# Kernel optimization log

Hardware: AMD Instinct MI355X
Metric: run time of the kernel (lower is better)

Reference implementation:

```python
import jax, jax.numpy as jnp
import numpy as np

B, N, DM = 4, 1024, 256
DEPTH, D_STATE, D_CONV, EXPAND = 12, 16, 4, 2
D_INNER = EXPAND * DM
DT_RANK = (DM + 15) // 16
MASKED = 256            # fixed number of masked tokens per row (CLS never masked)
MAX_VIS = N - MASKED    # static visible length -> jit-safe gather/pad
EPS = 1e-5


def setup_inputs() -> dict:
    key = jax.random.key(0)
    ks = jax.random.split(key, 8)
    tokens = jax.random.normal(ks[0], (B, N, DM), jnp.float32)
    # mask: exactly MASKED random positions True per row, among first N-1 (CLS visible)
    def row_mask(k):
        perm = jax.random.permutation(k, N - 1)
        return jnp.zeros((N,), bool).at[perm[:MASKED]].set(True)
    mask = jax.vmap(row_mask)(jax.random.split(ks[1], B))
    sc = 0.02
    L = DEPTH
    in_proj_w = jax.random.normal(ks[2], (L, 2 * D_INNER, DM), jnp.float32) * sc
    conv_w = jax.random.normal(ks[3], (L, D_INNER, D_CONV), jnp.float32) * sc
    conv_b = jnp.zeros((L, D_INNER), jnp.float32)
    x_proj_w = jax.random.normal(ks[4], (L, DT_RANK + 2 * D_STATE, D_INNER), jnp.float32) * sc
    dt_proj_w = jax.random.normal(ks[5], (L, D_INNER, DT_RANK), jnp.float32) * (DT_RANK ** -0.5)
    dt_proj_b = jnp.full((L, D_INNER), float(np.log(np.expm1(0.01))), jnp.float32)  # softplus^-1(0.01)
    A_log = jnp.log(jnp.broadcast_to(jnp.arange(1, D_STATE + 1, dtype=jnp.float32), (L, D_INNER, D_STATE)))
    D_skip = jnp.ones((L, D_INNER), jnp.float32)
    out_proj_w = jax.random.normal(ks[6], (L, DM, D_INNER), jnp.float32) * sc
    norm_w = jnp.ones((L, DM), jnp.float32)
    norm_f_w = jnp.ones((DM,), jnp.float32)
    ln_w = jnp.ones((DM,), jnp.float32)
    ln_b = jnp.zeros((DM,), jnp.float32)
    return dict(tokens=tokens, mask=mask, in_proj_w=in_proj_w, conv_w=conv_w, conv_b=conv_b,
                x_proj_w=x_proj_w, dt_proj_w=dt_proj_w, dt_proj_b=dt_proj_b, A_log=A_log,
                D_skip=D_skip, out_proj_w=out_proj_w, norm_w=norm_w, norm_f_w=norm_f_w,
                ln_w=ln_w, ln_b=ln_b)


def _rmsnorm(x, w):
    return x * jax.lax.rsqrt(jnp.mean(x * x, axis=-1, keepdims=True) + EPS) * w


def _selective_scan(dA, dBu, C):
    # linear recurrence h_t = dA_t * h_{t-1} + dBu_t via associative scan over time
    def comb(l, r):
        return (r[0] * l[0], r[0] * l[1] + r[1])
    _, h = jax.lax.associative_scan(comb, (dA, dBu), axis=1)  # [B,L,d_inner,d_state]
    return jnp.einsum('blds,bls->bld', h, C)


def _mamba(h, p):
    in_w, cw, cb, xw, dtw, dtb, Alog, Dd, ow = p
    L = h.shape[1]
    xz = jnp.einsum('bld,ed->ble', h, in_w)           # [B,L,2*d_inner]
    x, z = jnp.split(xz, 2, axis=-1)
    # causal depthwise conv1d (torch Conv1d, padding=d_conv-1, truncated to L)
    xp = jnp.pad(x, ((0, 0), (D_CONV - 1, 0), (0, 0)))
    x = sum(xp[:, k:k + L, :] * cw[:, k] for k in range(D_CONV)) + cb
    x = jax.nn.silu(x)
    xdbl = jnp.einsum('bld,ed->ble', x, xw)           # [B,L,dt_rank+2*d_state]
    dtr = xdbl[..., :DT_RANK]
    Bm = xdbl[..., DT_RANK:DT_RANK + D_STATE]
    Cm = xdbl[..., DT_RANK + D_STATE:]
    dt = jax.nn.softplus(jnp.einsum('blr,dr->bld', dtr, dtw) + dtb)  # [B,L,d_inner]
    A = -jnp.exp(Alog)                                 # [d_inner,d_state]
    dA = jnp.exp(dt[..., None] * A)                    # [B,L,d_inner,d_state]
    dBu = (dt * x)[..., None] * Bm[:, :, None, :]
    y = _selective_scan(dA, dBu, Cm) + Dd * x
    y = y * jax.nn.silu(z)
    return jnp.einsum('bld,od->blo', y, ow)


def _forward(tokens, mask, in_proj_w, conv_w, conv_b, x_proj_w, dt_proj_w, dt_proj_b,
             A_log, D_skip, out_proj_w, norm_w, norm_f_w, ln_w, ln_b):
    # gather visible tokens, preserving order (stable sort: visible first)
    sort_key = mask.astype(jnp.int32) * N + jnp.arange(N)
    order = jnp.argsort(sort_key, axis=1)[:, :MAX_VIS]           # [B,MAX_VIS]
    vis = jnp.take_along_axis(tokens, order[..., None], axis=1)  # [B,MAX_VIS,DM]

    def step(carry, p):
        hidden, residual = carry
        residual = hidden + residual
        hidden = _mamba(_rmsnorm(residual, p[0]), p[1:])
        return (hidden, residual), None

    layer_params = (norm_w, in_proj_w, conv_w, conv_b, x_proj_w, dt_proj_w, dt_proj_b,
                    A_log, D_skip, out_proj_w)
    (h, r), _ = jax.lax.scan(step, (vis, jnp.zeros_like(vis)), layer_params)
    h = _rmsnorm(h + r, norm_f_w)
    # final nn.LayerNorm
    mu = jnp.mean(h, axis=-1, keepdims=True)
    var = jnp.mean((h - mu) ** 2, axis=-1, keepdims=True)
    h = (h - mu) * jax.lax.rsqrt(var + EPS) * ln_w + ln_b
    return h[:, :-1], h[:, -1]


def reference(tokens, mask, in_proj_w, conv_w, conv_b, x_proj_w, dt_proj_w, dt_proj_b,
              A_log, D_skip, out_proj_w, norm_w, norm_f_w, ln_w, ln_b):
    return _forward(tokens, mask, in_proj_w, conv_w, conv_b, x_proj_w, dt_proj_w, dt_proj_b,
                    A_log, D_skip, out_proj_w, norm_w, norm_f_w, ln_w, ln_b)
```

## Files before the change

kernel.cpp:

```cpp
#include <hip/hip_runtime.h>
#include <stdint.h>

#define B_ 4
#define N_TOK 1024
#define DM 256
#define DEPTH 12
#define DSTATE 16
#define DIN 512
#define LVIS 768
#define MROWS (B_ * LVIS)
#define NCHUNK 64
#define CLEN 12
#define EPS_F 1e-5f
#define YS 520
#define AS_ 264
#define LOG2E 1.4426950408889634f
#define LN2   0.6931471805599453f

typedef __attribute__((ext_vector_type(8))) short s8v;
typedef __attribute__((ext_vector_type(4))) float f4v;

__device__ __forceinline__ float bs2f(uint32_t u) {
  uint32_t x = (u & 0xffffu) << 16;
  float f; __builtin_memcpy(&f, &x, 4); return f;
}
__device__ __forceinline__ uint16_t f2b(float f) {
  uint32_t u; __builtin_memcpy(&u, &f, 4);
  return (uint16_t)((u + 0x7fffu + ((u >> 16) & 1u)) >> 16);
}
__device__ __forceinline__ float exp2_f(float x) {
  float r; asm("v_exp_f32 %0, %1" : "=v"(r) : "v"(x)); return r;
}
__device__ __forceinline__ float log2_f(float x) {
  float r; asm("v_log_f32 %0, %1" : "=v"(r) : "v"(x)); return r;
}
__device__ __forceinline__ float rcp_f(float x) {
  float r; asm("v_rcp_f32 %0, %1" : "=v"(r) : "v"(x)); return r;
}
__device__ __forceinline__ float silu_f(float x) {
  return x * rcp_f(1.f + exp2_f(-x * LOG2E));
}
__device__ __forceinline__ float softplus_f(float x) {
  float t = exp2_f(-fabsf(x) * LOG2E);
  return fmaxf(x, 0.f) + log2_f(1.f + t) * LN2;
}
__device__ __forceinline__ float block_sum256(float v, volatile float* scr) {
  int t = threadIdx.x, lane = t & 63, wid = t >> 6;
#pragma unroll
  for (int o = 32; o > 0; o >>= 1) v += __shfl_down(v, o);
  __syncthreads();
  if (lane == 0) scr[wid] = v;
  __syncthreads();
  return scr[0] + scr[1] + scr[2] + scr[3];
}

__global__ void detect_kernel(const void* mask, const uint32_t* nf, int* flags) {
  __shared__ int cnt[3];
  int t = threadIdx.x;
  if (t < 3) cnt[t] = 0;
  __syncthreads();
  const uint32_t* pi = (const uint32_t*)mask;
  const uint16_t* ph = (const uint16_t*)mask;
  const uint8_t*  pb = (const uint8_t*)mask;
  int c32 = 0, cbf = 0, c8 = 0;
  for (int i = t; i < 1024; i += 256) {
    c32 += (pi[i] != 0u);
    cbf += (ph[i] != 0);
    c8  += (pb[i] != 0);
  }
  atomicAdd(&cnt[0], c32);
  atomicAdd(&cnt[1], cbf);
  atomicAdd(&cnt[2], c8);
  __syncthreads();
  if (t == 0) {
    int f;
    if (cnt[0] == 256) f = 0;
    else if (cnt[1] == 256) f = 2;
    else f = 1;
    flags[0] = f;
    flags[1] = (nf[0] == 0x3F800000u) ? 0 : 1;
  }
}

struct CvtArgs {
  const void* src[13];
  void*       dst[13];
  int         n[13];
  int         isb16[13];
};
__global__ __launch_bounds__(256) void cvt_all_kernel(CvtArgs a, int total,
                                                      const int* __restrict__ flags) {
  int e = blockIdx.x * 256 + threadIdx.x;
  if (e >= total) return;
  int i = 0;
  while (e >= a.n[i]) { e -= a.n[i]; ++i; }
  int srcb16 = flags[1];
  if (a.isb16[i]) {
    uint16_t v = srcb16 ? ((const uint16_t*)a.src[i])[e]
                        : f2b(((const float*)a.src[i])[e]);
    ((uint16_t*)a.dst[i])[e] = v;
  } else {
    float v = srcb16 ? bs2f(((const uint16_t*)a.src[i])[e])
                     : ((const float*)a.src[i])[e];
    ((float*)a.dst[i])[e] = v;
  }
}

__global__ __launch_bounds__(1024) void order_kernel(const void* mask,
                                                     const int* __restrict__ flags,
                                                     int* __restrict__ order) {
  int b = blockIdx.x, i = threadIdx.x;
  int f = flags[0];
  int mv;
  if (f == 0)      mv = (((const uint32_t*)mask)[b * N_TOK + i] != 0u);
  else if (f == 1) mv = (((const uint8_t*)mask)[b * N_TOK + i] != 0);
  else             mv = (((const uint16_t*)mask)[b * N_TOK + i] != 0);
  int vis = !mv;
  unsigned long long mb = __ballot(vis);
  int lane = i & 63, wid = i >> 6;
  int wpre = __popcll(mb & ((1ull << lane) - 1ull));
  __shared__ int wsum[16];
  __shared__ int woff[16];
  if (lane == 0) wsum[wid] = __popcll(mb);
  __syncthreads();
  if (i == 0) { int a = 0; for (int w = 0; w < 16; ++w) { woff[w] = a; a += wsum[w]; } }
  __syncthreads();
  if (vis) {
    int pos = woff[wid] + wpre;
    if (pos < LVIS) order[b * LVIS + pos] = i;
  }
}

__global__ __launch_bounds__(256) void gather_rms_kernel(const void* __restrict__ tokens,
                                                         const int* __restrict__ order,
                                                         const int* __restrict__ flags,
                                                         const float* __restrict__ nw,
                                                         float* __restrict__ residual,
                                                         uint16_t* __restrict__ rmsb16) {
  __shared__ float scr[4];
  int row = blockIdx.x;
  int b = row / LVIS;
  int d = threadIdx.x;
  int idx = order[row];
  size_t src = ((size_t)(b * N_TOK + idx)) * DM + d;
  float v = flags[1] ? bs2f(((const uint16_t*)tokens)[src]) : ((const float*)tokens)[src];
  size_t i = (size_t)row * DM + d;
  residual[i] = v;
  float ss = block_sum256(v * v, scr);
  rmsb16[i] = f2b(v * rsqrtf(ss / DM + EPS_F) * nw[d]);
}

__device__ __forceinline__ size_t cidx(int b, int c, int s, int d) {
  return (((size_t)(b * NCHUNK + c) * 16 + s)) * DIN + d;
}

__global__ __launch_bounds__(1024, 4) void scan1_kernel(
    const uint16_t* __restrict__ rmsb16, const uint16_t* __restrict__ inw,
    const uint16_t* __restrict__ xw,
    const float* __restrict__ cw, const float* __restrict__ cb,
    const float* __restrict__ dtw, const float* __restrict__ dtb,
    const float* __restrict__ Alog, const float* __restrict__ Dsk,
    uint16_t* __restrict__ xz16, float* __restrict__ hend,
    float* __restrict__ pend, float* __restrict__ xdbl_out,
    float* __restrict__ yloc, float* __restrict__ Ssum) {
  __shared__ uint16_t As[16 * AS_];
  __shared__ uint16_t xzl[16 * YS];
  __shared__ float red[8][768];
  __shared__ float xds[CLEN * 48];
  const int t = threadIdx.x;
  const int wv = t >> 6, lane = t & 63;
  const int lm = lane & 15, lq = lane >> 4;
  const int c = blockIdx.x & (NCHUNK - 1);
  const int b = blockIdx.x >> 6;
  const int rowbase = b * LVIS + c * CLEN;
  if (t < 512) {
    int r = t >> 5, seg = t & 31;
    int grow = rowbase - 3 + r;
    if (grow < 0) grow = 0;
    if (grow > MROWS - 1) grow = MROWS - 1;
    *(uint4*)(As + r * AS_ + seg * 8) =
        *(const uint4*)(rmsb16 + (size_t)grow * DM + seg * 8);
  }
  __syncthreads();
  {
    f4v acc[4];
#pragma unroll
    for (int j = 0; j < 4; ++j) acc[j] = (f4v){0.f, 0.f, 0.f, 0.f};
    for (int k0 = 0; k0 < DM; k0 += 32) {
      s8v a = *(const s8v*)(As + lm * AS_ + k0 + lq * 8);
#pragma unroll
      for (int j = 0; j < 4; ++j) {
        int n = (4 * wv + j) * 16 + lm;
        s8v bw = *(const s8v*)(inw + (size_t)n * DM + k0 + lq * 8);
        acc[j] = __builtin_amdgcn_mfma_f32_16x16x32_bf16(a, bw, acc[j], 0, 0, 0);
      }
    }
#pragma unroll
    for (int j = 0; j < 4; ++j) {
      int col = (4 * wv + j) * 16 + lm;
#pragma unroll
      for (int rr = 0; rr < 4; ++rr) {
        int tr = lq * 4 + rr;
        uint16_t v = f2b(acc[j][rr]);
        if (col < 512) xzl[tr * YS + col] = v;
        if (tr >= 3 && tr < 15)
          xz16[(size_t)(rowbase + tr - 3) * 1024 + col] = v;
      }
    }
  }
  __syncthreads();
  if (wv < 8) {
    f4v acc[3];
#pragma unroll
    for (int j = 0; j < 3; ++j) acc[j] = (f4v){0.f, 0.f, 0.f, 0.f};
    const int l = c * CLEN + lm;
    const bool t3 = l >= 3, t2 = l >= 2, t1 = l >= 1;
#pragma unroll
    for (int ki = 0; ki < 2; ++ki) {
      int kk = wv * 64 + ki * 32 + lq * 8;
      s8v a8 = {0, 0, 0, 0, 0, 0, 0, 0};
      if (lm < CLEN) {
        const s8v zv = {0, 0, 0, 0, 0, 0, 0, 0};
        s8v x0 = *(const s8v*)(xzl + (lm + 3) * YS + kk);
        s8v x1 = t1 ? *(const s8v*)(xzl + (lm + 2) * YS + kk) : zv;
        s8v x2 = t2 ? *(const s8v*)(xzl + (lm + 1) * YS + kk) : zv;
        s8v x3 = t3 ? *(const s8v*)(xzl + (lm + 0) * YS + kk) : zv;
#pragma unroll
        for (int j = 0; j < 8; ++j) {
          int ch = kk + j;
          float4 w = *(const float4*)(cw + ch * 4);
          float a = cb[ch] + bs2f((uint16_t)x3[j]) * w.x +
                    bs2f((uint16_t)x2[j]) * w.y +
                    bs2f((uint16_t)x1[j]) * w.z + bs2f((uint16_t)x0[j]) * w.w;
          a8[j] = (short)f2b(silu_f(a));
        }
      }
#pragma unroll
      for (int j = 0; j < 3; ++j) {
        s8v bb = *(const s8v*)(xw + (size_t)(j * 16 + lm) * DIN + kk);
        acc[j] = __builtin_amdgcn_mfma_f32_16x16x32_bf16(a8, bb, acc[j], 0, 0, 0);
      }
    }
#pragma unroll
    for (int j = 0; j < 3; ++j)
#pragma unroll
      for (int rr = 0; rr < 4; ++rr)
        red[wv][(lq * 4 + rr) * 48 + j * 16 + lm] = acc[j][rr];
  }
  __syncthreads();
  if (t < CLEN * 48) {
    float v = red[0][t] + red[1][t] + red[2][t] + red[3][t] +
              red[4][t] + red[5][t] + red[6][t] + red[7][t];
    xds[t] = v;
    xdbl_out[(size_t)(rowbase + t / 48) * 48 + (t % 48)] = v;
  }
  __syncthreads();
  if (t < DIN) {
    const int d = t;
    float A2[16], dw[16];
    {
      const float4* ap = (const float4*)(Alog + (size_t)d * 16);
      const float4* wp = (const float4*)(dtw + (size_t)d * 16);
#pragma unroll
      for (int q = 0; q < 4; ++q) {
        float4 a4 = ap[q], w4 = wp[q];
        A2[4 * q + 0] = -__expf(a4.x) * LOG2E;
        A2[4 * q + 1] = -__expf(a4.y) * LOG2E;
        A2[4 * q + 2] = -__expf(a4.z) * LOG2E;
        A2[4 * q + 3] = -__expf(a4.w) * LOG2E;
        dw[4 * q + 0] = w4.x; dw[4 * q + 1] = w4.y;
        dw[4 * q + 2] = w4.z; dw[4 * q + 3] = w4.w;
      }
    }
    float dtbv = dtb[d], cbv = cb[d], Dv = Dsk[d];
    float4 cwv = *(const float4*)(cw + d * 4);
    float w3 = 0.f, w2 = 0.f, w1 = 0.f;
    if (c > 0) {
      w3 = bs2f(xzl[0 * YS + d]);
      w2 = bs2f(xzl[1 * YS + d]);
      w1 = bs2f(xzl[2 * YS + d]);
    }
    float h[16];
#pragma unroll
    for (int s = 0; s < 16; ++s) h[s] = 0.f;
    float S = 0.f;
    for (int l = 0; l < CLEN; ++l) {
      float xn = bs2f(xzl[(l + 3) * YS + d]);
      float xv = silu_f(cbv + w3 * cwv.x + w2 * cwv.y + w1 * cwv.z + xn * cwv.w);
      w3 = w2; w2 = w1; w1 = xn;
      const float* xd = xds + l * 48;
      float dtraw = dtbv;
#pragma unroll
      for (int q = 0; q < 16; ++q) dtraw += xd[q] * dw[q];
      float dtv = softplus_f(dtraw);
      float dtx = dtv * xv;
      S += dtv;
      float y = 0.f;
#pragma unroll
      for (int s = 0; s < 16; ++s) {
        float dA = exp2_f(dtv * A2[s]);
        h[s] = dA * h[s] + dtx * xd[16 + s];
        y += h[s] * xd[32 + s];
      }
      size_t oi = (size_t)(rowbase + l) * DIN + d;
      yloc[oi] = y + Dv * xv;
      Ssum[oi] = S;
    }
#pragma unroll
    for (int s = 0; s < 16; ++s) {
      hend[cidx(b, c, s, d)] = h[s];
      pend[cidx(b, c, s, d)] = exp2_f(A2[s] * S);
    }
  }
}

__global__ __launch_bounds__(256) void scan2_kernel(const float* __restrict__ hend,
                                                    const float* __restrict__ pend,
                                                    float* __restrict__ hin) {
  __shared__ float sP[4 * 64];
  __shared__ float sE[4 * 64];
  int t = threadIdx.x;
  int w = t >> 6, lane = t & 63;
  int chain = blockIdx.x * 64 + lane;
  int d = chain & (DIN - 1);
  int s = (chain >> 9) & 15;
  int b = chain >> 13;
  float P = 1.f, E = 0.f;
  float pr[16], hr[16];
#pragma unroll
  for (int i = 0; i < 16; ++i) {
    size_t idx = cidx(b, w * 16 + i, s, d);
    float pv = pend[idx], ev = hend[idx];
    pr[i] = pv; hr[i] = ev;
    E = pv * E + ev;
    P *= pv;
  }
  sP[w * 64 + lane] = P;
  sE[w * 64 + lane] = E;
  __syncthreads();
  float hc = 0.f;
#pragma unroll
  for (int j = 0; j < 3; ++j)
    if (j < w) hc = sP[j * 64 + lane] * hc + sE[j * 64 + lane];
#pragma unroll
  for (int i = 0; i < 16; ++i) {
    hin[cidx(b, w * 16 + i, s, d)] = hc;
    hc = pr[i] * hc + hr[i];
  }
}

__global__ __launch_bounds__(1024, 4) void scan3_fused_kernel(
    const uint16_t* __restrict__ xz16, const float* __restrict__ xdbl,
    const float* __restrict__ Alog, const float* __restrict__ hin,
    const float* __restrict__ yloc, const float* __restrict__ Ssum,
    const uint16_t* __restrict__ W, const float* __restrict__ nw,
    float* __restrict__ residual, uint16_t* __restrict__ rmsb16) {
  __shared__ float xds[CLEN * 48];
  __shared__ uint16_t yml[16 * YS];
  __shared__ float part[16][16];
  __shared__ float scale[16];
  const int t = threadIdx.x;
  const int c = blockIdx.x & (NCHUNK - 1);
  const int b = blockIdx.x >> 6;
  const int rowbase = b * LVIS + c * CLEN;
  if (t < CLEN * 48)
    xds[t] = xdbl[(size_t)(rowbase + t / 48) * 48 + (t % 48)];
  for (int e = t; e < 4 * 512; e += 1024)
    yml[(12 + (e >> 9)) * YS + (e & 511)] = 0;
  __syncthreads();
  if (t < DIN) {
    const int d = t;
    float A2[16];
    {
      const float4* ap = (const float4*)(Alog + (size_t)d * 16);
#pragma unroll
      for (int q = 0; q < 4; ++q) {
        float4 a4 = ap[q];
        A2[4 * q + 0] = -__expf(a4.x) * LOG2E;
        A2[4 * q + 1] = -__expf(a4.y) * LOG2E;
        A2[4 * q + 2] = -__expf(a4.z) * LOG2E;
        A2[4 * q + 3] = -__expf(a4.w) * LOG2E;
      }
    }
    float chin[16];
#pragma unroll
    for (int s = 0; s < 16; ++s) chin[s] = hin[cidx(b, c, s, d)];
    for (int l = 0; l < CLEN; ++l) {
      int row = rowbase + l;
      size_t oi = (size_t)row * DIN + d;
      float S = Ssum[oi];
      float yl = yloc[oi];
      const float* xd = xds + l * 48;
      float carry = 0.f;
#pragma unroll
      for (int s = 0; s < 16; ++s)
        carry += xd[32 + s] * chin[s] * exp2_f(A2[s] * S);
      float zv = bs2f(xz16[(size_t)row * 1024 + 512 + d]);
      yml[l * YS + d] = f2b((yl + carry) * silu_f(zv));
    }
  }
  __syncthreads();
  {
    const int wv = t >> 6, lane = t & 63;
    const int lm = lane & 15, lq = lane >> 4;
    f4v acc = (f4v){0.f, 0.f, 0.f, 0.f};
    for (int k0 = 0; k0 < DIN; k0 += 32) {
      s8v a = *(const s8v*)(yml + lm * YS + k0 + lq * 8);
      int n = wv * 16 + lm;
      s8v bf = *(const s8v*)(W + (size_t)n * DIN + k0 + lq * 8);
      acc = __builtin_amdgcn_mfma_f32_16x16x32_bf16(a, bf, acc, 0, 0, 0);
    }
    float vv[4];
    float sum[4] = {0.f, 0.f, 0.f, 0.f};
#pragma unroll
    for (int rr = 0; rr < 4; ++rr) {
      int row = lq * 4 + rr;
      if (row < CLEN) {
        int col = wv * 16 + lm;
        float v = acc[rr] + residual[(size_t)(rowbase + row) * DM + col];
        vv[rr] = v;
        sum[rr] += v * v;
      }
    }
#pragma unroll
    for (int rr = 0; rr < 4; ++rr) {
#pragma unroll
      for (int o = 1; o < 16; o <<= 1) sum[rr] += __shfl_xor(sum[rr], o);
    }
    if (lm == 0) {
#pragma unroll
      for (int rr = 0; rr < 4; ++rr) {
        int row = lq * 4 + rr;
        if (row < 16) part[row][wv] = sum[rr];
      }
    }
    __syncthreads();
    if (t < CLEN) {
      float s = 0.f;
#pragma unroll
      for (int w = 0; w < 16; ++w) s += part[t][w];
      scale[t] = rsqrtf(s / DM + EPS_F);
    }
    __syncthreads();
#pragma unroll
    for (int rr = 0; rr < 4; ++rr) {
      int row = lq * 4 + rr;
      if (row < CLEN) {
        float sc = scale[row];
        int col = wv * 16 + lm;
        float v = vv[rr];
        size_t oi = (size_t)(rowbase + row) * DM + col;
        residual[oi] = v;
        rmsb16[oi] = f2b(v * sc * nw[col]);
      }
    }
  }
}

__global__ __launch_bounds__(256) void final_kernel(const float* __restrict__ residual,
                                                    const float* __restrict__ nfw,
                                                    const float* __restrict__ lnw,
                                                    const float* __restrict__ lnb,
                                                    const int* __restrict__ flags,
                                                    void* __restrict__ out) {
  __shared__ float scr[4];
  int row = blockIdx.x, d = threadIdx.x;
  size_t i = (size_t)row * DM + d;
  float v = residual[i];
  float ss = block_sum256(v * v, scr);
  float h = v * rsqrtf(ss / DM + EPS_F) * nfw[d];
  float mu = block_sum256(h, scr) / DM;
  float dv = h - mu;
  float var = block_sum256(dv * dv, scr) / DM;
  float o = dv * rsqrtf(var + EPS_F) * lnw[d] + lnb[d];
  int b = row / LVIS, l = row % LVIS;
  size_t oi = (l < LVIS - 1)
                ? ((size_t)(b * (LVIS - 1) + l) * DM + d)
                : ((size_t)B_ * (LVIS - 1) * DM + (size_t)b * DM + d);
  if (flags[1]) ((uint16_t*)out)[oi] = f2b(o);
  else          ((float*)out)[oi] = o;
}

extern "C" void kernel_launch(void* const* d_in, const int* in_sizes, int n_in,
                              void* d_out, int out_size, void* d_ws, size_t ws_size,
                              hipStream_t stream) {
  char* ws = (char*)d_ws;
  size_t off = 0;
  auto alloc = [&](size_t bytes) -> void* {
    void* p = ws + off;
    off += (bytes + 255) & ~(size_t)255;
    return p;
  };
  const int f32_idx[10] = {3, 4, 6, 7, 8, 9, 11, 12, 13, 14};
  const int b16_idx[3]  = {2, 5, 10};
  float*    f32c[15] = {nullptr};
  uint16_t* b16c[15] = {nullptr};
  for (int j = 0; j < 10; ++j) {
    int i = f32_idx[j];
    f32c[i] = (float*)alloc((size_t)in_sizes[i] * 4);
  }
  for (int j = 0; j < 3; ++j) {
    int i = b16_idx[j];
    b16c[i] = (uint16_t*)alloc((size_t)in_sizes[i] * 2);
  }
  float*    residual = (float*)alloc((size_t)MROWS * DM * 4);
  uint16_t* rmsb16   = (uint16_t*)alloc((size_t)MROWS * DM * 2);
  uint16_t* xz16     = (uint16_t*)alloc((size_t)MROWS * 1024 * 2);
  float*    xdbl     = (float*)alloc((size_t)MROWS * 48 * 4);
  float*    hend     = (float*)alloc((size_t)B_ * NCHUNK * DIN * 16 * 4);
  float*    pend     = (float*)alloc((size_t)B_ * NCHUNK * DIN * 16 * 4);
  float*    hin      = (float*)alloc((size_t)B_ * NCHUNK * DIN * 16 * 4);
  float*    yloc     = (float*)alloc((size_t)MROWS * DIN * 4);
  float*    Ssum     = (float*)alloc((size_t)MROWS * DIN * 4);
  int*      order    = (int*)alloc((size_t)B_ * LVIS * 4);
  int*      flags    = (int*)alloc(256);

  detect_kernel<<<1, 256, 0, stream>>>(d_in[1], (const uint32_t*)d_in[12], flags);

  CvtArgs ca;
  int total = 0, slot = 0;
  for (int j = 0; j < 3; ++j) {
    int i = b16_idx[j];
    ca.src[slot] = d_in[i]; ca.dst[slot] = b16c[i];
    ca.n[slot] = in_sizes[i]; ca.isb16[slot] = 1;
    total += in_sizes[i]; ++slot;
  }
  for (int j = 0; j < 10; ++j) {
    int i = f32_idx[j];
    ca.src[slot] = d_in[i]; ca.dst[slot] = f32c[i];
    ca.n[slot] = in_sizes[i]; ca.isb16[slot] = 0;
    total += in_sizes[i]; ++slot;
  }
  cvt_all_kernel<<<(total + 255) / 256, 256, 0, stream>>>(ca, total, flags);

  const uint16_t* in_w   = b16c[2];
  const float*    conv_w = f32c[3];
  const float*    conv_b = f32c[4];
  const uint16_t* x_w    = b16c[5];
  const float*    dt_w   = f32c[6];
  const float*    dt_b   = f32c[7];
  const float*    A_log  = f32c[8];
  const float*    D_skip = f32c[9];
  const uint16_t* out_w  = b16c[10];
  const float*    norm_w = f32c[11];
  const float*    norm_f = f32c[12];
  const float*    ln_w   = f32c[13];
  const float*    ln_b   = f32c[14];

  order_kernel<<<B_, 1024, 0, stream>>>(d_in[1], flags, order);
  gather_rms_kernel<<<MROWS, 256, 0, stream>>>(d_in[0], order, flags, norm_w,
                                               residual, rmsb16);

  for (int L = 0; L < DEPTH; ++L) {
    scan1_kernel<<<B_ * NCHUNK, 1024, 0, stream>>>(
        rmsb16, in_w + (size_t)L * 1024 * DM, x_w + (size_t)L * 48 * DIN,
        conv_w + (size_t)L * DIN * 4, conv_b + (size_t)L * DIN,
        dt_w + (size_t)L * DIN * 16, dt_b + (size_t)L * DIN,
        A_log + (size_t)L * DIN * 16, D_skip + (size_t)L * DIN,
        xz16, hend, pend, xdbl, yloc, Ssum);
    scan2_kernel<<<(B_ * 16 * DIN * 4) / 256, 256, 0, stream>>>(hend, pend, hin);
    int Lnext = (L + 1 < DEPTH) ? (L + 1) : L;
    scan3_fused_kernel<<<B_ * NCHUNK, 1024, 0, stream>>>(
        xz16, xdbl, A_log + (size_t)L * DIN * 16, hin, yloc, Ssum,
        out_w + (size_t)L * DM * DIN, norm_w + (size_t)Lnext * DM,
        residual, rmsb16);
  }

  final_kernel<<<MROWS, 256, 0, stream>>>(residual, norm_f, ln_w, ln_b,
                                          flags, d_out);
}
```

Measured before the change: 798.7 us.

## Split in-projection GEMM out of scan1 into a separate kernel with x/z halves

Moves the in_proj GEMM from the fused chunk-scan kernel into its own kernel, tiled over 16-row blocks and split into x and z halves written to separate buffers. The scan kernel now loads the x half with its 3-row halo from global memory and runs with 512 threads instead of 1024. This drops the redundant recomputation of the 3 halo rows per chunk and the wasted MFMA rows (16 computed for 12 used). It also lets the GEMM and the scan use different block shapes. In exchange it adds one more launch per layer and a round trip of x through global memory.

```diff
diff --git a/kernel.cpp b/kernel.cpp
--- a/kernel.cpp
+++ b/kernel.cpp
@@ -154,18 +154,60 @@
   return (((size_t)(b * NCHUNK + c) * 16 + s)) * DIN + d;
 }
 
-__global__ __launch_bounds__(1024, 4) void scan1_kernel(
+__global__ __launch_bounds__(512, 4) void inproj_kernel(
     const uint16_t* __restrict__ rmsb16, const uint16_t* __restrict__ inw,
-    const uint16_t* __restrict__ xw,
+    uint16_t* __restrict__ xh16, uint16_t* __restrict__ zh16) {
+  __shared__ uint16_t As[16 * AS_];
+  __shared__ uint16_t xt[16 * YS];
+  const int t = threadIdx.x;
+  const int wv = t >> 6, lane = t & 63;
+  const int lm = lane & 15, lq = lane >> 4;
+  const int hf = blockIdx.x & 1;
+  const int row0 = (blockIdx.x >> 1) * 16;
+  {
+    int r = t >> 5, seg = t & 31;
+    *(uint4*)(As + r * AS_ + seg * 8) =
+        *(const uint4*)(rmsb16 + (size_t)(row0 + r) * DM + seg * 8);
+  }
+  __syncthreads();
+  f4v acc[4];
+#pragma unroll
+  for (int j = 0; j < 4; ++j) acc[j] = (f4v){0.f, 0.f, 0.f, 0.f};
+  for (int k0 = 0; k0 < DM; k0 += 32) {
+    s8v a = *(const s8v*)(As + lm * AS_ + k0 + lq * 8);
+#pragma unroll
+    for (int j = 0; j < 4; ++j) {
+      int n = hf * 512 + (4 * wv + j) * 16 + lm;
+      s8v bw = *(const s8v*)(inw + (size_t)n * DM + k0 + lq * 8);
+      acc[j] = __builtin_amdgcn_mfma_f32_16x16x32_bf16(a, bw, acc[j], 0, 0, 0);
+    }
+  }
+#pragma unroll
+  for (int j = 0; j < 4; ++j) {
+    int col = (4 * wv + j) * 16 + lm;
+#pragma unroll
+    for (int rr = 0; rr < 4; ++rr)
+      xt[(lq * 4 + rr) * YS + col] = f2b(acc[j][rr]);
+  }
+  __syncthreads();
+  uint16_t* dst = hf ? zh16 : xh16;
+  for (int e = t; e < 1024; e += 512) {
+    int r = e >> 6, q = e & 63;
+    *(uint4*)(dst + (size_t)(row0 + r) * 512 + q * 8) =
+        *(const uint4*)(xt + r * YS + q * 8);
+  }
+}
+
+__global__ __launch_bounds__(512, 4) void scanS_kernel(
+    const uint16_t* __restrict__ xh16, const uint16_t* __restrict__ xw,
     const float* __restrict__ cw, const float* __restrict__ cb,
     const float* __restrict__ dtw, const float* __restrict__ dtb,
     const float* __restrict__ Alog, const float* __restrict__ Dsk,
-    uint16_t* __restrict__ xz16, float* __restrict__ hend,
-    float* __restrict__ pend, float* __restrict__ xdbl_out,
-    float* __restrict__ yloc, float* __restrict__ Ssum) {
-  __shared__ uint16_t As[16 * AS_];
-  __shared__ uint16_t xzl[16 * YS];
-  __shared__ float red[8][768];
+    float* __restrict__ hend, float* __restrict__ pend,
+    float* __restrict__ xdbl_out, float* __restrict__ yloc,
+    float* __restrict__ Ssum) {
+  __shared__ uint16_t xh[16 * YS];
+  __shared__ float red[8][CLEN * 48];
   __shared__ float xds[CLEN * 48];
   const int t = threadIdx.x;
   const int wv = t >> 6, lane = t & 63;
@@ -173,43 +215,16 @@
   const int c = blockIdx.x & (NCHUNK - 1);
   const int b = blockIdx.x >> 6;
   const int rowbase = b * LVIS + c * CLEN;
-  if (t < 512) {
-    int r = t >> 5, seg = t & 31;
+  for (int e = t; e < 16 * 64; e += 512) {
+    int r = e >> 6, q = e & 63;
     int grow = rowbase - 3 + r;
     if (grow < 0) grow = 0;
     if (grow > MROWS - 1) grow = MROWS - 1;
-    *(uint4*)(As + r * AS_ + seg * 8) =
-        *(const uint4*)(rmsb16 + (size_t)grow * DM + seg * 8);
+    *(uint4*)(xh + r * YS + q * 8) =
+        *(const uint4*)(xh16 + (size_t)grow * 512 + q * 8);
   }
   __syncthreads();
   {
-    f4v acc[4];
-#pragma unroll
-    for (int j = 0; j < 4; ++j) acc[j] = (f4v){0.f, 0.f, 0.f, 0.f};
-    for (int k0 = 0; k0 < DM; k0 += 32) {
-      s8v a = *(const s8v*)(As + lm * AS_ + k0 + lq * 8);
-#pragma unroll
-      for (int j = 0; j < 4; ++j) {
-        int n = (4 * wv + j) * 16 + lm;
-        s8v bw = *(const s8v*)(inw + (size_t)n * DM + k0 + lq * 8);
-        acc[j] = __builtin_amdgcn_mfma_f32_16x16x32_bf16(a, bw, acc[j], 0, 0, 0);
-      }
-    }
-#pragma unroll
-    for (int j = 0; j < 4; ++j) {
-      int col = (4 * wv + j) * 16 + lm;
-#pragma unroll
-      for (int rr = 0; rr < 4; ++rr) {
-        int tr = lq * 4 + rr;
-        uint16_t v = f2b(acc[j][rr]);
-        if (col < 512) xzl[tr * YS + col] = v;
-        if (tr >= 3 && tr < 15)
-          xz16[(size_t)(rowbase + tr - 3) * 1024 + col] = v;
-      }
-    }
-  }
-  __syncthreads();
-  if (wv < 8) {
     f4v acc[3];
 #pragma unroll
     for (int j = 0; j < 3; ++j) acc[j] = (f4v){0.f, 0.f, 0.f, 0.f};
@@ -221,10 +236,10 @@
       s8v a8 = {0, 0, 0, 0, 0, 0, 0, 0};
       if (lm < CLEN) {
         const s8v zv = {0, 0, 0, 0, 0, 0, 0, 0};
-        s8v x0 = *(const s8v*)(xzl + (lm + 3) * YS + kk);
-        s8v x1 = t1 ? *(const s8v*)(xzl + (lm + 2) * YS + kk) : zv;
-        s8v x2 = t2 ? *(const s8v*)(xzl + (lm + 1) * YS + kk) : zv;
-        s8v x3 = t3 ? *(const s8v*)(xzl + (lm + 0) * YS + kk) : zv;
+        s8v x0 = *(const s8v*)(xh + (lm + 3) * YS + kk);
+        s8v x1 = t1 ? *(const s8v*)(xh + (lm + 2) * YS + kk) : zv;
+        s8v x2 = t2 ? *(const s8v*)(xh + (lm + 1) * YS + kk) : zv;
+        s8v x3 = t3 ? *(const s8v*)(xh + (lm + 0) * YS + kk) : zv;
 #pragma unroll
         for (int j = 0; j < 8; ++j) {
           int ch = kk + j;
@@ -248,14 +263,14 @@
         red[wv][(lq * 4 + rr) * 48 + j * 16 + lm] = acc[j][rr];
   }
   __syncthreads();
-  if (t < CLEN * 48) {
-    float v = red[0][t] + red[1][t] + red[2][t] + red[3][t] +
-              red[4][t] + red[5][t] + red[6][t] + red[7][t];
-    xds[t] = v;
-    xdbl_out[(size_t)(rowbase + t / 48) * 48 + (t % 48)] = v;
-  }
-  __syncthreads();
-  if (t < DIN) {
+  for (int e = t; e < CLEN * 48; e += 512) {
+    float v = red[0][e] + red[1][e] + red[2][e] + red[3][e] +
+              red[4][e] + red[5][e] + red[6][e] + red[7][e];
+    xds[e] = v;
+    xdbl_out[(size_t)(rowbase + e / 48) * 48 + (e % 48)] = v;
+  }
+  __syncthreads();
+  {
     const int d = t;
     float A2[16], dw[16];
     {
@@ -276,16 +291,16 @@
     float4 cwv = *(const float4*)(cw + d * 4);
     float w3 = 0.f, w2 = 0.f, w1 = 0.f;
     if (c > 0) {
-      w3 = bs2f(xzl[0 * YS + d]);
-      w2 = bs2f(xzl[1 * YS + d]);
-      w1 = bs2f(xzl[2 * YS + d]);
+      w3 = bs2f(xh[0 * YS + d]);
+      w2 = bs2f(xh[1 * YS + d]);
+      w1 = bs2f(xh[2 * YS + d]);
     }
     float h[16];
 #pragma unroll
     for (int s = 0; s < 16; ++s) h[s] = 0.f;
     float S = 0.f;
     for (int l = 0; l < CLEN; ++l) {
-      float xn = bs2f(xzl[(l + 3) * YS + d]);
+      float xn = bs2f(xh[(l + 3) * YS + d]);
       float xv = silu_f(cbv + w3 * cwv.x + w2 * cwv.y + w1 * cwv.z + xn * cwv.w);
       w3 = w2; w2 = w1; w1 = xn;
       const float* xd = xds + l * 48;
@@ -350,7 +365,7 @@
 }
 
 __global__ __launch_bounds__(1024, 4) void scan3_fused_kernel(
-    const uint16_t* __restrict__ xz16, const float* __restrict__ xdbl,
+    const uint16_t* __restrict__ zh16, const float* __restrict__ xdbl,
     const float* __restrict__ Alog, const float* __restrict__ hin,
     const float* __restrict__ yloc, const float* __restrict__ Ssum,
     const uint16_t* __restrict__ W, const float* __restrict__ nw,
@@ -395,7 +410,7 @@
 #pragma unroll
       for (int s = 0; s < 16; ++s)
         carry += xd[32 + s] * chin[s] * exp2_f(A2[s] * S);
-      float zv = bs2f(xz16[(size_t)row * 1024 + 512 + d]);
+      float zv = bs2f(zh16[(size_t)row * 512 + d]);
       yml[l * YS + d] = f2b((yl + carry) * silu_f(zv));
     }
   }
@@ -505,7 +520,8 @@
   }
   float*    residual = (float*)alloc((size_t)MROWS * DM * 4);
   uint16_t* rmsb16   = (uint16_t*)alloc((size_t)MROWS * DM * 2);
-  uint16_t* xz16     = (uint16_t*)alloc((size_t)MROWS * 1024 * 2);
+  uint16_t* xh16     = (uint16_t*)alloc((size_t)MROWS * 512 * 2);
+  uint16_t* zh16     = (uint16_t*)alloc((size_t)MROWS * 512 * 2);
   float*    xdbl     = (float*)alloc((size_t)MROWS * 48 * 4);
   float*    hend     = (float*)alloc((size_t)B_ * NCHUNK * DIN * 16 * 4);
   float*    pend     = (float*)alloc((size_t)B_ * NCHUNK * DIN * 16 * 4);
@@ -552,16 +568,18 @@
                                                residual, rmsb16);
 
   for (int L = 0; L < DEPTH; ++L) {
-    scan1_kernel<<<B_ * NCHUNK, 1024, 0, stream>>>(
-        rmsb16, in_w + (size_t)L * 1024 * DM, x_w + (size_t)L * 48 * DIN,
+    inproj_kernel<<<(MROWS / 16) * 2, 512, 0, stream>>>(
+        rmsb16, in_w + (size_t)L * 1024 * DM, xh16, zh16);
+    scanS_kernel<<<B_ * NCHUNK, 512, 0, stream>>>(
+        xh16, x_w + (size_t)L * 48 * DIN,
         conv_w + (size_t)L * DIN * 4, conv_b + (size_t)L * DIN,
         dt_w + (size_t)L * DIN * 16, dt_b + (size_t)L * DIN,
         A_log + (size_t)L * DIN * 16, D_skip + (size_t)L * DIN,
-        xz16, hend, pend, xdbl, yloc, Ssum);
+        hend, pend, xdbl, yloc, Ssum);
     scan2_kernel<<<(B_ * 16 * DIN * 4) / 256, 256, 0, stream>>>(hend, pend, hin);
     int Lnext = (L + 1 < DEPTH) ? (L + 1) : L;
     scan3_fused_kernel<<<B_ * NCHUNK, 1024, 0, stream>>>(
-        xz16, xdbl, A_log + (size_t)L * DIN * 16, hin, yloc, Ssum,
+        zh16, xdbl, A_log + (size_t)L * DIN * 16, hin, yloc, Ssum,
         out_w + (size_t)L * DM * DIN, norm_w + (size_t)Lnext * DM,
         residual, rmsb16);
   }
```

Result: slower. 823.4 us (+3.1%).
